# Performance work log

Measured on AMD Instinct MI355X. Metric: run time of the kernel, lower is better.

Reference implementation:

```python
import jax, jax.numpy as jnp
import numpy as np

B, N, D = 32768, 256, 3


def setup_inputs() -> dict:
    key = jax.random.key(0)
    k1, k2 = jax.random.split(key)
    keypoints = jax.random.normal(k1, (B, N, D), dtype=jnp.float32)
    perm = jax.random.permutation(k2, B)  # emulates torch.randperm, deterministic
    return {"keypoints": keypoints, "perm": perm}


def _transform_a2b(src, dst):
    # src, dst: [B, N, 3]; batched similarity (Umeyama/Kabsch-style) alignment.
    num = src.shape[1]
    src_mean = src.mean(axis=1)                     # [B, 3]
    dst_mean = dst.mean(axis=1)                     # [B, 3]
    src_d = src - src_mean[:, None]                 # [B, N, 3]
    dst_d = dst - dst_mean[:, None]                 # [B, N, 3]
    A = jnp.einsum('bni,bnj->bij', dst_d, src_d) / num  # [B, 3, 3] covariance
    U, S, Vt = jnp.linalg.svd(A)
    # NOTE: in the original torch code `d[neg_A][:, -1, -1] = -1` writes into a
    # COPY (advanced indexing), so d stays identity for all batches. We
    # faithfully reproduce that actual behavior: R = U @ V^T, scale uses sum(S).
    var_sum = jnp.mean(jnp.sum(src_d * src_d, axis=-1), axis=1)  # sum of per-dim biased var
    scale = jnp.sum(S, axis=-1) / var_sum           # [B]
    R = U @ Vt                                      # [B, 3, 3]
    T = dst_mean - scale[:, None] * jnp.einsum('bij,bj->bi', R, src_mean)  # [B, 3]
    # Original computes R, scale, T under torch.no_grad().
    R = jax.lax.stop_gradient(R)
    scale = jax.lax.stop_gradient(scale)
    T = jax.lax.stop_gradient(T)
    return src @ (jnp.swapaxes(R, -1, -2) * scale[:, None, None]) + T[:, None]


def reference(keypoints, perm):
    dst = keypoints[perm]                            # randomized keypoints
    trans = _transform_a2b(keypoints, dst)
    return jnp.mean(jnp.abs(trans - dst))
```

## Files before the change

kernel.cpp:

```cpp
#include <hip/hip_runtime.h>
#include <math.h>

#define GEO_N 256

__device__ __forceinline__ float frcp(float x) { return __builtin_amdgcn_rcpf(x); }
__device__ __forceinline__ float frsq(float x) { return __builtin_amdgcn_rsqf(x); }
__device__ __forceinline__ float fsqrtf_(float x) { return __builtin_amdgcn_sqrtf(x); }

__device__ __forceinline__ float wredf(float v) {
#pragma unroll
  for (int off = 32; off; off >>= 1) v += __shfl_xor(v, off, 64);
  return v;
}

__device__ __forceinline__ void eigvec3(float g00, float g01, float g02,
                                        float g11, float g12, float g22,
                                        float l, float v[3]) {
  const float m00 = g00 - l, m11 = g11 - l, m22 = g22 - l;
  const float a0 = g01 * g12 - g02 * m11, a1 = g02 * g01 - m00 * g12, a2 = m00 * m11 - g01 * g01;
  const float b0 = g01 * m22 - g02 * g12, b1 = g02 * g02 - m00 * m22, b2 = m00 * g12 - g01 * g02;
  const float c0 = m11 * m22 - g12 * g12, c1 = g12 * g02 - g01 * m22, c2 = g01 * g12 - m11 * g02;
  const float na = a0 * a0 + a1 * a1 + a2 * a2;
  const float nb = b0 * b0 + b1 * b1 + b2 * b2;
  const float nc = c0 * c0 + c1 * c1 + c2 * c2;
  float s0 = a0, s1 = a1, s2 = a2, ns = na;
  if (nb > ns) { s0 = b0; s1 = b1; s2 = b2; ns = nb; }
  if (nc > ns) { s0 = c0; s1 = c1; s2 = c2; ns = nc; }
  const bool bad = ns < 1e-28f;
  const float inv = frsq(fmaxf(ns, 1e-28f));
  v[0] = bad ? 1.0f : s0 * inv;
  v[1] = bad ? 0.0f : s1 * inv;
  v[2] = bad ? 0.0f : s2 * inv;
}

__device__ __forceinline__ void solve_rst(const float s0in[16], float bc[13]) {
  const float invN = 1.0f / (float)GEO_N;
  const float smx = s0in[0] * invN, smy = s0in[1] * invN, smz = s0in[2] * invN;
  const float dmx = s0in[3] * invN, dmy = s0in[4] * invN, dmz = s0in[5] * invN;
  const float A00 = s0in[6] * invN - dmx * smx,  A01 = s0in[7] * invN - dmx * smy,  A02 = s0in[8] * invN - dmx * smz;
  const float A10 = s0in[9] * invN - dmy * smx,  A11 = s0in[10] * invN - dmy * smy, A12 = s0in[11] * invN - dmy * smz;
  const float A20 = s0in[12] * invN - dmz * smx, A21 = s0in[13] * invN - dmz * smy, A22 = s0in[14] * invN - dmz * smz;
  const float var_sum = s0in[15] * invN - (smx * smx + smy * smy + smz * smz);

  const float g00 = A00 * A00 + A10 * A10 + A20 * A20;
  const float g11 = A01 * A01 + A11 * A11 + A21 * A21;
  const float g22 = A02 * A02 + A12 * A12 + A22 * A22;
  const float g01 = A00 * A01 + A10 * A11 + A20 * A21;
  const float g02 = A00 * A02 + A10 * A12 + A20 * A22;
  const float g12 = A01 * A02 + A11 * A12 + A21 * A22;

  const float q = (g00 + g11 + g22) * (1.0f / 3.0f);
  const float c00 = g00 - q, c11 = g11 - q, c22 = g22 - q;
  const float p1 = g01 * g01 + g02 * g02 + g12 * g12;
  const float p2 = c00 * c00 + c11 * c11 + c22 * c22 + 2.0f * p1;
  const float p = fsqrtf_(p2 * (1.0f / 6.0f));
  const float pinv = frcp(fmaxf(p, 1e-20f));
  const float detC = c00 * (c11 * c22 - g12 * g12)
                   - g01 * (g01 * c22 - g12 * g02)
                   + g02 * (g01 * g12 - c11 * g02);
  float rr = 0.5f * detC * pinv * pinv * pinv;
  rr = fminf(1.0f, fmaxf(-1.0f, rr));
  const float arr = fabsf(rr);
  const float acs = fsqrtf_(fmaxf(1.0f - arr, 0.0f)) *
      (1.5707288f + arr * (-0.2121144f + arr * (0.0742610f + arr * (-0.0187293f))));
  const float acr = (rr >= 0.0f) ? acs : (3.14159265f - acs);
  const float phi = acr * (1.0f / 3.0f);
  const float x1 = phi * phi;
  const float cph = 1.0f + x1 * (-0.5f + x1 * ((1.0f / 24.0f) - x1 * (1.0f / 720.0f)));
  const float uu = 1.04719755f - phi;
  const float x2 = uu * uu;
  const float cp3 = -(1.0f + x2 * (-0.5f + x2 * ((1.0f / 24.0f) - x2 * (1.0f / 720.0f))));
  const float l0 = q + 2.0f * p * cph;
  const float l2 = q + 2.0f * p * cp3;
  const float l1 = 3.0f * q - l0 - l2;

  float v0[3], v2[3];
  eigvec3(g00, g01, g02, g11, g12, g22, l0, v0);
  eigvec3(g00, g01, g02, g11, g12, g22, l2, v2);

  const float sg0 = fsqrtf_(fmaxf(l0, 0.0f));
  const float sg1 = fsqrtf_(fmaxf(l1, 0.0f));
  const float sg2 = fsqrtf_(fmaxf(l2, 0.0f));
  const float iv0 = (sg0 > 1e-20f) ? frcp(sg0) : 0.0f;
  const float iv1 = (sg1 > 1e-20f) ? frcp(sg1) : 0.0f;
  const float iv2 = (sg2 > 1e-20f) ? frcp(sg2) : 0.0f;

  const float da = iv0 - iv1, db = iv2 - iv1;
  const float w00 = iv1 + da * v0[0] * v0[0] + db * v2[0] * v2[0];
  const float w11 = iv1 + da * v0[1] * v0[1] + db * v2[1] * v2[1];
  const float w22 = iv1 + da * v0[2] * v0[2] + db * v2[2] * v2[2];
  const float w01 = da * v0[0] * v0[1] + db * v2[0] * v2[1];
  const float w02 = da * v0[0] * v0[2] + db * v2[0] * v2[2];
  const float w12 = da * v0[1] * v0[2] + db * v2[1] * v2[2];

  const float R00 = A00 * w00 + A01 * w01 + A02 * w02;
  const float R01 = A00 * w01 + A01 * w11 + A02 * w12;
  const float R02 = A00 * w02 + A01 * w12 + A02 * w22;
  const float R10 = A10 * w00 + A11 * w01 + A12 * w02;
  const float R11 = A10 * w01 + A11 * w11 + A12 * w12;
  const float R12 = A10 * w02 + A11 * w12 + A12 * w22;
  const float R20 = A20 * w00 + A21 * w01 + A22 * w02;
  const float R21 = A20 * w01 + A21 * w11 + A22 * w12;
  const float R22 = A20 * w02 + A21 * w12 + A22 * w22;

  const float scale = (sg0 + sg1 + sg2) * frcp(fmaxf(var_sum, 1e-30f));
  bc[0] = R00; bc[1] = R01; bc[2] = R02;
  bc[3] = R10; bc[4] = R11; bc[5] = R12;
  bc[6] = R20; bc[7] = R21; bc[8] = R22;
  bc[9] = scale;
  bc[10] = dmx - scale * (R00 * smx + R01 * smy + R02 * smz);
  bc[11] = dmy - scale * (R10 * smx + R11 * smy + R12 * smz);
  bc[12] = dmz - scale * (R20 * smx + R21 * smy + R22 * smz);
}

__global__ __launch_bounds__(256) void geo_wave4p(const float* __restrict__ kp,
                                                  const int* __restrict__ perm,
                                                  float* __restrict__ partials,
                                                  int B, int NW) {
  const int wid = (blockIdx.x << 2) | (threadIdx.x >> 6);
  if (wid >= NW) return;
  const int lane = threadIdx.x & 63;
  const int b0 = wid * 4;
  const float4* base = (const float4*)kp;

  int pm[4];
#pragma unroll
  for (int i = 0; i < 4; ++i) pm[i] = perm[min(b0 + i, B - 1)];

  float4 S[4][3], D[4][3];
  float parked = 0.0f;

#define GEO_LOAD(i)                                                        \
  {                                                                        \
    const int bb = min(b0 + (i), B - 1);                                   \
    const float4* s4 = base + (size_t)bb * 192 + lane * 3;                 \
    const float4* d4 = base + (size_t)pm[(i)] * 192 + lane * 3;            \
    S[(i)][0] = s4[0]; S[(i)][1] = s4[1]; S[(i)][2] = s4[2];               \
    D[(i)][0] = d4[0]; D[(i)][1] = d4[1]; D[(i)][2] = d4[2];               \
  }

#define GEO_MOM(i)                                                         \
  {                                                                        \
    const float s_[12] = {S[(i)][0].x, S[(i)][0].y, S[(i)][0].z, S[(i)][0].w, \
                          S[(i)][1].x, S[(i)][1].y, S[(i)][1].z, S[(i)][1].w, \
                          S[(i)][2].x, S[(i)][2].y, S[(i)][2].z, S[(i)][2].w}; \
    const float d_[12] = {D[(i)][0].x, D[(i)][0].y, D[(i)][0].z, D[(i)][0].w, \
                          D[(i)][1].x, D[(i)][1].y, D[(i)][1].z, D[(i)][1].w, \
                          D[(i)][2].x, D[(i)][2].y, D[(i)][2].z, D[(i)][2].w}; \
    float r[16];                                                           \
    _Pragma("unroll") for (int k = 0; k < 16; ++k) r[k] = 0.0f;            \
    _Pragma("unroll") for (int p = 0; p < 4; ++p) {                        \
      const float sx = s_[3 * p + 0], sy = s_[3 * p + 1], sz = s_[3 * p + 2]; \
      const float dx = d_[3 * p + 0], dy = d_[3 * p + 1], dz = d_[3 * p + 2]; \
      r[0] += sx; r[1] += sy; r[2] += sz;                                  \
      r[3] += dx; r[4] += dy; r[5] += dz;                                  \
      r[6] += dx * sx; r[7] += dx * sy; r[8] += dx * sz;                   \
      r[9] += dy * sx; r[10] += dy * sy; r[11] += dy * sz;                 \
      r[12] += dz * sx; r[13] += dz * sy; r[14] += dz * sz;                \
      r[15] += sx * sx + sy * sy + sz * sz;                                \
    }                                                                      \
    const int b1 = lane & 1, b2 = (lane >> 1) & 1, b3 = (lane >> 2) & 1, b4 = (lane >> 3) & 1; \
    float v8[8], v4_[4], v2_[2], v1;                                       \
    _Pragma("unroll") for (int k = 0; k < 8; ++k) {                        \
      float send = b1 ? r[k] : r[k + 8];                                   \
      float recv = __shfl_xor(send, 1, 64);                                \
      v8[k] = (b1 ? r[k + 8] : r[k]) + recv;                               \
    }                                                                      \
    _Pragma("unroll") for (int k = 0; k < 4; ++k) {                        \
      float send = b2 ? v8[k] : v8[k + 4];                                 \
      float recv = __shfl_xor(send, 2, 64);                                \
      v4_[k] = (b2 ? v8[k + 4] : v8[k]) + recv;                            \
    }                                                                      \
    _Pragma("unroll") for (int k = 0; k < 2; ++k) {                        \
      float send = b3 ? v4_[k] : v4_[k + 2];                               \
      float recv = __shfl_xor(send, 4, 64);                                \
      v2_[k] = (b3 ? v4_[k + 2] : v4_[k]) + recv;                          \
    }                                                                      \
    {                                                                      \
      float send = b4 ? v2_[0] : v2_[1];                                   \
      float recv = __shfl_xor(send, 8, 64);                                \
      v1 = (b4 ? v2_[1] : v2_[0]) + recv;                                  \
    }                                                                      \
    v1 += __shfl_xor(v1, 16, 64);                                          \
    v1 += __shfl_xor(v1, 32, 64);                                          \
    if ((lane >> 4) == (i)) parked = v1;                                   \
  }

  GEO_LOAD(0)
  GEO_LOAD(1)
  __builtin_amdgcn_sched_barrier(0);
  GEO_MOM(0)
  GEO_LOAD(2)
  __builtin_amdgcn_sched_barrier(0);
  GEO_MOM(1)
  GEO_LOAD(3)
  __builtin_amdgcn_sched_barrier(0);
  GEO_MOM(2)
  __builtin_amdgcn_sched_barrier(0);
  GEO_MOM(3)

#undef GEO_LOAD
#undef GEO_MOM

  constexpr int br[16] = {0, 8, 4, 12, 2, 10, 6, 14, 1, 9, 5, 13, 3, 11, 7, 15};
  float s0[16];
#pragma unroll
  for (int k = 0; k < 16; ++k)
    s0[k] = __shfl(parked, ((lane & 3) << 4) | br[k], 64);

  float bc[13];
  solve_rst(s0, bc);

  float acc = 0.0f;
#pragma unroll
  for (int i = 0; i < 4; ++i) {
    const float R00 = __shfl(bc[0], i, 64), R01 = __shfl(bc[1], i, 64), R02 = __shfl(bc[2], i, 64);
    const float R10 = __shfl(bc[3], i, 64), R11 = __shfl(bc[4], i, 64), R12 = __shfl(bc[5], i, 64);
    const float R20 = __shfl(bc[6], i, 64), R21 = __shfl(bc[7], i, 64), R22 = __shfl(bc[8], i, 64);
    const float sc  = __shfl(bc[9], i, 64);
    const float Tx  = __shfl(bc[10], i, 64), Ty = __shfl(bc[11], i, 64), Tz = __shfl(bc[12], i, 64);
    const float s[12] = {S[i][0].x, S[i][0].y, S[i][0].z, S[i][0].w,
                         S[i][1].x, S[i][1].y, S[i][1].z, S[i][1].w,
                         S[i][2].x, S[i][2].y, S[i][2].z, S[i][2].w};
    const float d[12] = {D[i][0].x, D[i][0].y, D[i][0].z, D[i][0].w,
                         D[i][1].x, D[i][1].y, D[i][1].z, D[i][1].w,
                         D[i][2].x, D[i][2].y, D[i][2].z, D[i][2].w};
    float a = 0.0f;
#pragma unroll
    for (int q = 0; q < 4; ++q) {
      const float sx = s[3 * q + 0], sy = s[3 * q + 1], sz = s[3 * q + 2];
      const float dx = d[3 * q + 0], dy = d[3 * q + 1], dz = d[3 * q + 2];
      const float e0 = sc * (R00 * sx + R01 * sy + R02 * sz) + Tx - dx;
      const float e1 = sc * (R10 * sx + R11 * sy + R12 * sz) + Ty - dy;
      const float e2 = sc * (R20 * sx + R21 * sy + R22 * sz) + Tz - dz;
      a += fabsf(e0) + fabsf(e1) + fabsf(e2);
    }
    if (b0 + i < B) acc += a;
  }
  acc = wredf(acc);
  if (lane == 0) partials[wid] = acc;
}

__global__ __launch_bounds__(1024) void geo_fin(const float* __restrict__ partials,
                                                float* __restrict__ out, int n,
                                                double inv_total) {
  const int t = threadIdx.x;
  double acc = 0.0;
  for (int i = t; i < n; i += 1024) acc += (double)partials[i];
#pragma unroll
  for (int off = 32; off; off >>= 1) acc += __shfl_xor(acc, off, 64);
  __shared__ double sred[16];
  if ((t & 63) == 0) sred[t >> 6] = acc;
  __syncthreads();
  if (t == 0) {
    double tot = 0.0;
#pragma unroll
    for (int k = 0; k < 16; ++k) tot += sred[k];
    out[0] = (float)(tot * inv_total);
  }
}

extern "C" void kernel_launch(void* const* d_in, const int* in_sizes, int n_in,
                              void* d_out, int out_size, void* d_ws, size_t ws_size,
                              hipStream_t stream) {
  const float* kp = (const float*)d_in[0];
  const int* perm = (const int*)d_in[1];
  float* out = (float*)d_out;
  const int B = in_sizes[1];
  const double inv_total = 1.0 / ((double)B * (double)GEO_N * 3.0);

  const int NW = (B + 3) / 4;
  float* partials = (float*)d_ws;
  const int grid = (NW + 3) / 4;
  geo_wave4p<<<grid, 256, 0, stream>>>(kp, perm, partials, B, NW);
  geo_fin<<<1, 1024, 0, stream>>>(partials, out, NW, inv_total);
}
```

Before: 39.77 us.

## Fuse final reduction into main kernel via last-block atomic counter

Removes the separate finalize kernel launch. Each block now reduces its four waves in shared memory, writes one partial, and increments an atomic counter; the last block to finish sums all partials and writes the output. It also loads the four perm indices with a single int4 load and drops one scheduling barrier. The cost is a memset launch per call for the counter, plus threadfence and atomic overhead in every block.

```diff
diff --git a/kernel.cpp b/kernel.cpp
--- a/kernel.cpp
+++ b/kernel.cpp
@@ -113,19 +113,26 @@
   bc[12] = dmz - scale * (R20 * smx + R21 * smy + R22 * smz);
 }
 
-__global__ __launch_bounds__(256) void geo_wave4p(const float* __restrict__ kp,
+__global__ __launch_bounds__(256) void geo_wave4f(const float* __restrict__ kp,
                                                   const int* __restrict__ perm,
                                                   float* __restrict__ partials,
-                                                  int B, int NW) {
-  const int wid = (blockIdx.x << 2) | (threadIdx.x >> 6);
-  if (wid >= NW) return;
-  const int lane = threadIdx.x & 63;
+                                                  unsigned int* __restrict__ counter,
+                                                  float* __restrict__ out,
+                                                  int B, int NW, double inv_total) {
+  const int w = threadIdx.x >> 6, lane = threadIdx.x & 63;
+  const int wid0 = blockIdx.x * 4 + w;
+  const int wid = min(wid0, NW - 1);
   const int b0 = wid * 4;
   const float4* base = (const float4*)kp;
 
   int pm[4];
-#pragma unroll
-  for (int i = 0; i < 4; ++i) pm[i] = perm[min(b0 + i, B - 1)];
+  if ((B & 3) == 0 && b0 + 3 < B) {
+    const int4 pv = *(const int4*)(perm + b0);
+    pm[0] = pv.x; pm[1] = pv.y; pm[2] = pv.z; pm[3] = pv.w;
+  } else {
+#pragma unroll
+    for (int i = 0; i < 4; ++i) pm[i] = perm[min(b0 + i, B - 1)];
+  }
 
   float4 S[4][3], D[4][3];
   float parked = 0.0f;
@@ -196,7 +203,6 @@
   GEO_LOAD(3)
   __builtin_amdgcn_sched_barrier(0);
   GEO_MOM(2)
-  __builtin_amdgcn_sched_barrier(0);
   GEO_MOM(3)
 
 #undef GEO_LOAD
@@ -235,28 +241,34 @@
       const float e2 = sc * (R20 * sx + R21 * sy + R22 * sz) + Tz - dz;
       a += fabsf(e0) + fabsf(e1) + fabsf(e2);
     }
-    if (b0 + i < B) acc += a;
+    if (wid0 < NW && (size_t)wid0 * 4 + i < (size_t)B) acc += a;
   }
   acc = wredf(acc);
-  if (lane == 0) partials[wid] = acc;
-}
-
-__global__ __launch_bounds__(1024) void geo_fin(const float* __restrict__ partials,
-                                                float* __restrict__ out, int n,
-                                                double inv_total) {
-  const int t = threadIdx.x;
-  double acc = 0.0;
-  for (int i = t; i < n; i += 1024) acc += (double)partials[i];
-#pragma unroll
-  for (int off = 32; off; off >>= 1) acc += __shfl_xor(acc, off, 64);
-  __shared__ double sred[16];
-  if ((t & 63) == 0) sred[t >> 6] = acc;
+
+  __shared__ float lred[4];
+  __shared__ unsigned int islast;
+  if (lane == 0) lred[w] = acc;
   __syncthreads();
-  if (t == 0) {
-    double tot = 0.0;
-#pragma unroll
-    for (int k = 0; k < 16; ++k) tot += sred[k];
-    out[0] = (float)(tot * inv_total);
+  if (threadIdx.x == 0) {
+    partials[blockIdx.x] = (lred[0] + lred[1]) + (lred[2] + lred[3]);
+    __threadfence();
+    const unsigned int old = atomicAdd(counter, 1u);
+    islast = (old == gridDim.x - 1) ? 1u : 0u;
+  }
+  __syncthreads();
+
+  if (islast) {
+    __threadfence();
+    const int n = gridDim.x;
+    double dacc = 0.0;
+    for (int i = threadIdx.x; i < n; i += 256) dacc += (double)partials[i];
+#pragma unroll
+    for (int off = 32; off; off >>= 1) dacc += __shfl_xor(dacc, off, 64);
+    __shared__ double sred[4];
+    if (lane == 0) sred[w] = dacc;
+    __syncthreads();
+    if (threadIdx.x == 0)
+      out[0] = (float)(((sred[0] + sred[1]) + (sred[2] + sred[3])) * inv_total);
   }
 }
 
@@ -270,8 +282,11 @@
   const double inv_total = 1.0 / ((double)B * (double)GEO_N * 3.0);
 
   const int NW = (B + 3) / 4;
+  const int grid = (NW + 3) / 4;
   float* partials = (float*)d_ws;
-  const int grid = (NW + 3) / 4;
-  geo_wave4p<<<grid, 256, 0, stream>>>(kp, perm, partials, B, NW);
-  geo_fin<<<1, 1024, 0, stream>>>(partials, out, NW, inv_total);
-}
+  unsigned int* counter = (unsigned int*)(partials + grid);
+
+  hipMemsetAsync(counter, 0, sizeof(unsigned int), stream);
+  geo_wave4f<<<grid, 256, 0, stream>>>(kp, perm, partials, counter, out,
+                                       B, NW, inv_total);
+}
```

Measured after the change: 94.64 us. 2.38x slower.
